# Kernel tuning notes

Hardware: AMD Instinct MI355X
Metric: run time of the kernel (lower is better)

## Reference

```python
import jax, jax.numpy as jnp
import numpy as np

EPS = 1e-5

def setup_inputs() -> dict:
    key = jax.random.key(0)
    ks = jax.random.split(key, 8)
    N, C, ST, LT = 32, 2048, 16, 400
    ALPHA, K, BETA, CK = 4, 3, 4, 3
    Cb = C // BETA
    inp = {
        'st_feat': jax.random.normal(ks[0], (N, C, ST, 1, 1), dtype=jnp.float32),
        'lt_feat': jax.random.normal(ks[1], (N, C, LT, 1, 1), dtype=jnp.float32),
        # global branch G: Linear(ST->ST*alpha) -> BN1d -> ReLU -> Linear(->K) -> softmax
        'g_w1': jax.random.normal(ks[2], (ST * ALPHA, ST), dtype=jnp.float32) * 0.02,
        'g_bn_gamma': jnp.ones((ST * ALPHA,), jnp.float32),
        'g_bn_beta': jnp.zeros((ST * ALPHA,), jnp.float32),
        'g_bn_mean': jnp.zeros((ST * ALPHA,), jnp.float32),
        'g_bn_var': jnp.ones((ST * ALPHA,), jnp.float32),
        'g_w2': jax.random.normal(ks[3], (K, ST * ALPHA), dtype=jnp.float32) * 0.02,
        # local branch L: Conv1d(C->C/beta,k=3) -> BN1d -> ReLU -> Conv1d(C/beta->C,1) -> sigmoid
        'l_w1': jax.random.normal(ks[4], (Cb, C, CK), dtype=jnp.float32) * 0.02,
        'l_bn_gamma': jnp.ones((Cb,), jnp.float32),
        'l_bn_beta': jnp.zeros((Cb,), jnp.float32),
        'l_bn_mean': jnp.zeros((Cb,), jnp.float32),
        'l_bn_var': jnp.ones((Cb,), jnp.float32),
        'l_w2': jax.random.normal(ks[5], (C, Cb), dtype=jnp.float32) * 0.02,
    }
    return inp


def reference(st_feat, lt_feat, g_w1, g_bn_gamma, g_bn_beta, g_bn_mean, g_bn_var,
              g_w2, l_w1, l_bn_gamma, l_bn_beta, l_bn_mean, l_bn_var, l_w2):
    N, C, ST = st_feat.shape[:3]
    LT = lt_feat.shape[2]
    K = g_w2.shape[0]
    PAD = 1  # adaptive_convolution_padding; stride = 1
    # ---- global branch: per-(n,c) adaptive kernel (h=w=1 so avgpool is identity)
    st = st_feat.reshape(N * C, ST)                               # [NC, ST]
    h = st @ g_w1.T                                               # [NC, ST*alpha]
    h = (h - g_bn_mean) * jax.lax.rsqrt(g_bn_var + EPS) * g_bn_gamma + g_bn_beta
    h = jax.nn.relu(h)
    conv_kernel = jax.nn.softmax(h @ g_w2.T, axis=-1)             # [NC, K]
    # ---- local branch: channel-temporal sigmoid gate
    lt = lt_feat.reshape(N, C, LT)                                # [N, C, LT]
    x = jax.lax.conv_general_dilated(lt, l_w1, window_strides=(1,),
                                     padding=[(1, 1)],
                                     dimension_numbers=('NCH', 'OIH', 'NCH'))  # [N, C/beta, LT]
    x = (x - l_bn_mean[None, :, None]) * jax.lax.rsqrt(l_bn_var + EPS)[None, :, None] \
        * l_bn_gamma[None, :, None] + l_bn_beta[None, :, None]
    x = jax.nn.relu(x)
    gate = jax.nn.sigmoid(jnp.einsum('oc,nct->not', l_w2, x))     # [N, C, LT]
    new_lt = lt * gate
    # ---- temporal adaptive aggregation: per-(n,c) depthwise 1D conv, K taps
    kern = conv_kernel.reshape(N, C, K)
    xp = jnp.pad(new_lt, ((0, 0), (0, 0), (PAD, PAD)))            # [N, C, LT+2*PAD]
    out_len = LT + 2 * PAD - K + 1                                # == LT for K=3, PAD=1
    out = jnp.zeros((N, C, out_len), dtype=new_lt.dtype)
    for i in range(K):  # K is tiny (3)
        out = out + kern[:, :, i:i + 1] * xp[:, :, i:i + out_len]
    return out.reshape(N, C, out_len, 1, 1)
```

## Files before the change

### kernel.cpp

```cpp
#include <hip/hip_runtime.h>
#include <hip/hip_bf16.h>

#define N_   32
#define C_   2048
#define ST_  16
#define H_   64
#define K_   3
#define CB_  512
#define LT_  400
#define LTP_ 402
#define BK   32
#define TV1  254

using bf16x8 = __attribute__((ext_vector_type(8))) __bf16;
using f32x4  = __attribute__((ext_vector_type(4))) float;
typedef unsigned short ushort_t;

__device__ __forceinline__ unsigned short f2bf(float f) {
    unsigned int u = __float_as_uint(f);
    u = (u + 0x7fffu + ((u >> 16) & 1u)) >> 16;
    return (unsigned short)u;
}
__device__ __forceinline__ float bf2f(unsigned short h) {
    return __uint_as_float(((unsigned int)h) << 16);
}
__device__ __forceinline__ void gload16(const ushort_t* g, ushort_t* l) {
    __builtin_amdgcn_global_load_lds(
        (const __attribute__((address_space(1))) unsigned int*)g,
        (__attribute__((address_space(3))) unsigned int*)l, 16, 0, 0);
}

__global__ __launch_bounds__(256) void k_global(
    const float* __restrict__ st, const float* __restrict__ g_w1,
    const float* __restrict__ gam, const float* __restrict__ bet,
    const float* __restrict__ mean, const float* __restrict__ var,
    const float* __restrict__ g_w2, float* __restrict__ kern) {
    __shared__ float w1[H_][ST_];
    __shared__ float sc[H_], bi[H_];
    __shared__ float w2[K_][H_];
    int tid = threadIdx.x;
    for (int i = tid; i < H_ * ST_; i += 256) w1[i / ST_][i % ST_] = g_w1[i];
    if (tid < H_) {
        float s = gam[tid] * rsqrtf(var[tid] + 1e-5f);
        sc[tid] = s;
        bi[tid] = bet[tid] - mean[tid] * s;
    }
    for (int i = tid; i < K_ * H_; i += 256) w2[i / H_][i % H_] = g_w2[i];
    __syncthreads();
    int row = blockIdx.x * 256 + tid;
    const float* p = st + (size_t)row * ST_;
    float s[ST_];
#pragma unroll
    for (int i = 0; i < ST_; ++i) s[i] = p[i];
    float lg0 = 0.f, lg1 = 0.f, lg2 = 0.f;
    for (int j = 0; j < H_; ++j) {
        float h = 0.f;
#pragma unroll
        for (int i = 0; i < ST_; ++i) h = fmaf(w1[j][i], s[i], h);
        h = fmaxf(fmaf(h, sc[j], bi[j]), 0.f);
        lg0 = fmaf(w2[0][j], h, lg0);
        lg1 = fmaf(w2[1][j], h, lg1);
        lg2 = fmaf(w2[2][j], h, lg2);
    }
    float m = fmaxf(lg0, fmaxf(lg1, lg2));
    float e0 = __expf(lg0 - m), e1 = __expf(lg1 - m), e2 = __expf(lg2 - m);
    float inv = 1.f / (e0 + e1 + e2);
    float4 o = make_float4(e0 * inv, e1 * inv, e2 * inv, 0.f);
    *(float4*)(kern + (size_t)row * 4) = o;
}

__global__ __launch_bounds__(256) void k_transpose(
    const float* __restrict__ lt, ushort_t* __restrict__ ltT) {
    __shared__ float tile[32][33];
    int tt0 = blockIdx.x * 32;
    int cc  = blockIdx.y * 32;
    int n   = blockIdx.z;
    const float* src = lt + ((size_t)n * C_ + cc) * LT_;
    int tx = threadIdx.x & 31, ty = threadIdx.x >> 5;
#pragma unroll
    for (int i = 0; i < 4; ++i) {
        int c = ty + i * 8;
        int t = tt0 + tx;
        tile[c][tx] = (t < LT_) ? src[(size_t)c * LT_ + t] : 0.f;
    }
    __syncthreads();
    int cx  = (threadIdx.x & 15) * 2;
    int tyw = threadIdx.x >> 4;
    unsigned int* dst = (unsigned int*)(ltT + (size_t)n * LTP_ * C_ + cc + cx);
#pragma unroll
    for (int i = 0; i < 2; ++i) {
        int tl = tyw + i * 16;
        int t = tt0 + tl;
        if (t < LT_) {
            unsigned int v = (unsigned int)f2bf(tile[cx][tl]) |
                             ((unsigned int)f2bf(tile[cx + 1][tl]) << 16);
            dst[(size_t)(t + 1) * (C_ / 2)] = v;
        }
    }
}

__global__ __launch_bounds__(256) void k_zero(ushort_t* __restrict__ ltT) {
    int i = blockIdx.x * 256 + threadIdx.x;
    int n = i >> 11, c = i & (C_ - 1);
    size_t base = (size_t)n * LTP_ * C_;
    ltT[base + c] = 0;
    ltT[base + (size_t)(LTP_ - 1) * C_ + c] = 0;
}

__global__ __launch_bounds__(256) void k_w1(
    const float* __restrict__ l_w1, ushort_t* __restrict__ w1b) {
    int i = blockIdx.x * 256 + threadIdx.x;
    float a = l_w1[(size_t)i * 3 + 0];
    float b = l_w1[(size_t)i * 3 + 1];
    float c = l_w1[(size_t)i * 3 + 2];
    w1b[0 * (size_t)CB_ * C_ + i] = f2bf(a);
    w1b[1 * (size_t)CB_ * C_ + i] = f2bf(b);
    w1b[2 * (size_t)CB_ * C_ + i] = f2bf(c);
}

__global__ __launch_bounds__(256) void k_w2(
    const float* __restrict__ l_w2, ushort_t* __restrict__ w2b) {
    int i = blockIdx.x * 256 + threadIdx.x;
    w2b[i] = f2bf(l_w2[i]);
}

__global__ __launch_bounds__(512, 2) void k_gemm1(
    const ushort_t* __restrict__ ltT, const ushort_t* __restrict__ w1b,
    const float* __restrict__ bn_g, const float* __restrict__ bn_b,
    const float* __restrict__ bn_m, const float* __restrict__ bn_v,
    ushort_t* __restrict__ Xws) {
    __shared__ __align__(16) ushort_t Asm[3 * 256 * BK + 2 * BK];
    __shared__ __align__(16) ushort_t Bsm[3 * 384 * BK];
    const int tid = threadIdx.x;
    const int mseg = blockIdx.x;
    const int n   = mseg >> 1;
    const int tm  = (mseg & 1) * TV1;
    const int cb0 = blockIdx.y * 128;
    const int lane = tid & 63, lrow = lane & 15, quad = lane >> 4;
    const int wv = tid >> 6;
    const int wvM = wv >> 1, wvN = wv & 1;

    const int srow = lane >> 2;
    const int csrc = (((lane & 3) ^ ((lane >> 3) & 3)) << 3);
    const ushort_t* gA[2];
#pragma unroll
    for (int i = 0; i < 2; ++i) {
        int r = (2 * wv + i) * 16 + srow;
        int gr = tm + r; gr = gr < LTP_ - 1 ? gr : LTP_ - 1;
        gA[i] = ltT + ((size_t)n * LTP_ + gr) * C_ + csrc;
    }
    const ushort_t* gB[3];
#pragma unroll
    for (int j = 0; j < 3; ++j) {
        int rB = (3 * wv + j) * 16 + srow;
        gB[j] = w1b + ((size_t)((rB >> 7) * CB_ + cb0 + (rB & 127))) * C_ + csrc;
    }
    const int sB = lrow * BK + ((quad ^ ((lrow >> 1) & 3)) << 3);
    int sA[3];
#pragma unroll
    for (int k = 0; k < 3; ++k)
        sA[k] = (lrow + k) * BK + ((quad ^ (((lrow + k) >> 1) & 3)) << 3);

    f32x4 acc[4][4];
#pragma unroll
    for (int i = 0; i < 4; ++i)
#pragma unroll
        for (int j = 0; j < 4; ++j) acc[i][j] = (f32x4){0.f, 0.f, 0.f, 0.f};

#define STAGE1(buf)                                                         \
    {                                                                       \
        ushort_t* ad = Asm + (buf) * (256 * BK) + (2 * wv) * (16 * BK);     \
        gload16(gA[0], ad);                                                 \
        gload16(gA[1], ad + 16 * BK);                                       \
        gA[0] += BK; gA[1] += BK;                                           \
        ushort_t* bd = Bsm + (buf) * (384 * BK) + (3 * wv) * (16 * BK);     \
        gload16(gB[0], bd);                                                 \
        gload16(gB[1], bd + 16 * BK);                                       \
        gload16(gB[2], bd + 32 * BK);                                       \
        gB[0] += BK; gB[1] += BK; gB[2] += BK;                              \
    }

    STAGE1(0);
    STAGE1(1);
    int cur = 0, pre = 2;
    for (int s = 0; s < C_ / BK; ++s) {
        if (s < C_ / BK - 1) asm volatile("s_waitcnt vmcnt(5)" ::: "memory");
        else                 asm volatile("s_waitcnt vmcnt(0)" ::: "memory");
        __builtin_amdgcn_sched_barrier(0);
        __builtin_amdgcn_s_barrier();
        __builtin_amdgcn_sched_barrier(0);
        if (s < C_ / BK - 2) {
            STAGE1(pre);
            pre = (pre == 2) ? 0 : pre + 1;
        }
        const ushort_t* Ab = Asm + cur * (256 * BK) + wvM * (64 * BK);
        const ushort_t* Bb = Bsm + cur * (384 * BK) + wvN * (64 * BK) + sB;
        bf16x8 bfr[3][4];
#pragma unroll
        for (int k = 0; k < 3; ++k)
#pragma unroll
            for (int nf = 0; nf < 4; ++nf)
                bfr[k][nf] = *(const bf16x8*)(Bb + k * (128 * BK) + nf * (16 * BK));
        __builtin_amdgcn_s_setprio(1);
#pragma unroll
        for (int mf = 0; mf < 4; ++mf) {
            bf16x8 af[3];
#pragma unroll
            for (int k = 0; k < 3; ++k)
                af[k] = *(const bf16x8*)(Ab + sA[k] + mf * (16 * BK));
#pragma unroll
            for (int nf = 0; nf < 4; ++nf)
#pragma unroll
                for (int k = 0; k < 3; ++k)
                    acc[mf][nf] = __builtin_amdgcn_mfma_f32_16x16x32_bf16(af[k], bfr[k][nf], acc[mf][nf], 0, 0, 0);
        }
        __builtin_amdgcn_s_setprio(0);
        cur = (cur == 2) ? 0 : cur + 1;
    }
#undef STAGE1
    float sc[4], bo[4];
#pragma unroll
    for (int nf = 0; nf < 4; ++nf) {
        int cb = cb0 + wvN * 64 + nf * 16 + lrow;
        float s0 = bn_g[cb] * rsqrtf(bn_v[cb] + 1e-5f);
        sc[nf] = s0;
        bo[nf] = bn_b[cb] - bn_m[cb] * s0;
    }
#pragma unroll
    for (int mf = 0; mf < 4; ++mf) {
#pragma unroll
        for (int r = 0; r < 4; ++r) {
            int local = wvM * 64 + mf * 16 + quad * 4 + r;
            int t = tm + local;
            if (local < TV1 && t < LT_) {
#pragma unroll
                for (int nf = 0; nf < 4; ++nf) {
                    int cb = cb0 + wvN * 64 + nf * 16 + lrow;
                    float v = fmaxf(fmaf(acc[mf][nf][r], sc[nf], bo[nf]), 0.f);
                    Xws[((size_t)n * LT_ + t) * CB_ + cb] = f2bf(v);
                }
            }
        }
    }
}

__global__ __launch_bounds__(256, 3) void k_gemm2(
    const ushort_t* __restrict__ Xws, const ushort_t* __restrict__ w2b,
    ushort_t* __restrict__ gate) {
    __shared__ __align__(16) ushort_t Asm[3 * 128 * BK];
    __shared__ __align__(16) ushort_t Bsm[3 * 128 * BK];
    const int tid = threadIdx.x;
    const int cm  = blockIdx.x * 128;
    const int fn0 = blockIdx.y * 128;
    const int lane = tid & 63, lrow = lane & 15, quad = lane >> 4;
    const int wv = tid >> 6, wvM = wv & 1, wvN = wv >> 1;

    const int srow = lane >> 2;
    const int csrc = (((lane & 3) ^ ((lane >> 3) & 3)) << 3);
    const ushort_t* gA[2];
    const ushort_t* gB[2];
#pragma unroll
    for (int i = 0; i < 2; ++i) {
        int r = (2 * wv + i) * 16 + srow;
        gA[i] = w2b + (size_t)(cm + r) * CB_ + csrc;
        gB[i] = Xws + (size_t)(fn0 + r) * CB_ + csrc;
    }
    const int sOff = lrow * BK + ((quad ^ ((lrow >> 1) & 3)) << 3);

    f32x4 acc[4][4];
#pragma unroll
    for (int i = 0; i < 4; ++i)
#pragma unroll
        for (int j = 0; j < 4; ++j) acc[i][j] = (f32x4){0.f, 0.f, 0.f, 0.f};

#define STAGE2(buf)                                                         \
    {                                                                       \
        ushort_t* ad = Asm + (buf) * (128 * BK) + (2 * wv) * (16 * BK);     \
        ushort_t* bd = Bsm + (buf) * (128 * BK) + (2 * wv) * (16 * BK);     \
        gload16(gA[0], ad);                                                 \
        gload16(gA[1], ad + 16 * BK);                                       \
        gload16(gB[0], bd);                                                 \
        gload16(gB[1], bd + 16 * BK);                                       \
        gA[0] += BK; gA[1] += BK; gB[0] += BK; gB[1] += BK;                 \
    }

    STAGE2(0);
    STAGE2(1);
    int cur = 0, pre = 2;
    for (int s = 0; s < CB_ / BK; ++s) {
        if (s < CB_ / BK - 1) asm volatile("s_waitcnt vmcnt(4)" ::: "memory");
        else                  asm volatile("s_waitcnt vmcnt(0)" ::: "memory");
        __builtin_amdgcn_sched_barrier(0);
        __builtin_amdgcn_s_barrier();
        __builtin_amdgcn_sched_barrier(0);
        if (s < CB_ / BK - 2) {
            STAGE2(pre);
            pre = (pre == 2) ? 0 : pre + 1;
        }
        const ushort_t* Ab = Asm + cur * (128 * BK) + wvM * (64 * BK) + sOff;
        const ushort_t* Bb = Bsm + cur * (128 * BK) + wvN * (64 * BK) + sOff;
        bf16x8 af[4], bfm[4];
#pragma unroll
        for (int mf = 0; mf < 4; ++mf)
            af[mf] = *(const bf16x8*)(Ab + mf * (16 * BK));
#pragma unroll
        for (int nf = 0; nf < 4; ++nf)
            bfm[nf] = *(const bf16x8*)(Bb + nf * (16 * BK));
        __builtin_amdgcn_s_setprio(1);
#pragma unroll
        for (int mf = 0; mf < 4; ++mf)
#pragma unroll
            for (int nf = 0; nf < 4; ++nf)
                acc[mf][nf] = __builtin_amdgcn_mfma_f32_16x16x32_bf16(af[mf], bfm[nf], acc[mf][nf], 0, 0, 0);
        __builtin_amdgcn_s_setprio(0);
        cur = (cur == 2) ? 0 : cur + 1;
    }
#undef STAGE2
#pragma unroll
    for (int mf = 0; mf < 4; ++mf) {
#pragma unroll
        for (int r = 0; r < 4; ++r) {
            int c = cm + wvM * 64 + mf * 16 + quad * 4 + r;
#pragma unroll
            for (int nf = 0; nf < 4; ++nf) {
                unsigned fn = fn0 + wvN * 64 + nf * 16 + lrow;
                unsigned nn = fn / LT_;
                unsigned t  = fn - nn * LT_;
                float g = 1.f / (1.f + __expf(-acc[mf][nf][r]));
                gate[((size_t)nn * C_ + c) * LT_ + t] = f2bf(g);
            }
        }
    }
}

__global__ __launch_bounds__(256) void k_final(
    const float* __restrict__ lt, const ushort_t* __restrict__ gate,
    const float* __restrict__ kern, float* __restrict__ out) {
    long long idx = (long long)blockIdx.x * 256 + threadIdx.x;
    int t0 = (int)(idx % 50) * 8;
    long long nc = idx / 50;
    const float*    ltp = lt   + (size_t)nc * LT_;
    const ushort_t* gp  = gate + (size_t)nc * LT_;
    float4 kv = *(const float4*)(kern + (size_t)nc * 4);
    float4 va = *(const float4*)(ltp + t0);
    float4 vb = *(const float4*)(ltp + t0 + 4);
    float lm = (t0 > 0) ? ltp[t0 - 1] : 0.f;
    float lp = (t0 + 8 < LT_) ? ltp[t0 + 8] : 0.f;
    uint2 ga = *(const uint2*)(gp + t0);
    uint2 gb = *(const uint2*)(gp + t0 + 4);
    unsigned short gm = (t0 > 0) ? gp[t0 - 1] : (unsigned short)0;
    unsigned short gq = (t0 + 8 < LT_) ? gp[t0 + 8] : (unsigned short)0;
    float nl[10];
    nl[0] = lm   * bf2f(gm);
    nl[1] = va.x * bf2f((unsigned short)(ga.x & 0xffffu));
    nl[2] = va.y * bf2f((unsigned short)(ga.x >> 16));
    nl[3] = va.z * bf2f((unsigned short)(ga.y & 0xffffu));
    nl[4] = va.w * bf2f((unsigned short)(ga.y >> 16));
    nl[5] = vb.x * bf2f((unsigned short)(gb.x & 0xffffu));
    nl[6] = vb.y * bf2f((unsigned short)(gb.x >> 16));
    nl[7] = vb.z * bf2f((unsigned short)(gb.y & 0xffffu));
    nl[8] = vb.w * bf2f((unsigned short)(gb.y >> 16));
    nl[9] = lp   * bf2f(gq);
    float4 o0, o1;
    o0.x = kv.x * nl[0] + kv.y * nl[1] + kv.z * nl[2];
    o0.y = kv.x * nl[1] + kv.y * nl[2] + kv.z * nl[3];
    o0.z = kv.x * nl[2] + kv.y * nl[3] + kv.z * nl[4];
    o0.w = kv.x * nl[3] + kv.y * nl[4] + kv.z * nl[5];
    o1.x = kv.x * nl[4] + kv.y * nl[5] + kv.z * nl[6];
    o1.y = kv.x * nl[5] + kv.y * nl[6] + kv.z * nl[7];
    o1.z = kv.x * nl[6] + kv.y * nl[7] + kv.z * nl[8];
    o1.w = kv.x * nl[7] + kv.y * nl[8] + kv.z * nl[9];
    *(float4*)(out + (size_t)nc * LT_ + t0) = o0;
    *(float4*)(out + (size_t)nc * LT_ + t0 + 4) = o1;
}

extern "C" void kernel_launch(void* const* d_in, const int* in_sizes, int n_in,
                              void* d_out, int out_size, void* d_ws, size_t ws_size,
                              hipStream_t stream) {
    const float* st   = (const float*)d_in[0];
    const float* lt   = (const float*)d_in[1];
    const float* g_w1 = (const float*)d_in[2];
    const float* g_bg = (const float*)d_in[3];
    const float* g_bb = (const float*)d_in[4];
    const float* g_bm = (const float*)d_in[5];
    const float* g_bv = (const float*)d_in[6];
    const float* g_w2 = (const float*)d_in[7];
    const float* l_w1 = (const float*)d_in[8];
    const float* l_bg = (const float*)d_in[9];
    const float* l_bb = (const float*)d_in[10];
    const float* l_bm = (const float*)d_in[11];
    const float* l_bv = (const float*)d_in[12];
    const float* l_w2 = (const float*)d_in[13];
    float* out = (float*)d_out;

    char* ws = (char*)d_ws;
    float*    kern = (float*)(ws + 0);
    ushort_t* w1b  = (ushort_t*)(ws + 1048576);
    ushort_t* w2b  = (ushort_t*)(ws + 7340032);
    ushort_t* Xws  = (ushort_t*)(ws + 9437184);
    ushort_t* ltT  = (ushort_t*)(ws + 22544384);
    ushort_t* gate = ltT;

    k_global<<<dim3((N_ * C_) / 256), dim3(256), 0, stream>>>(
        st, g_w1, g_bg, g_bb, g_bm, g_bv, g_w2, kern);
    k_w1<<<dim3((CB_ * C_) / 256), dim3(256), 0, stream>>>(l_w1, w1b);
    k_w2<<<dim3((C_ * CB_) / 256), dim3(256), 0, stream>>>(l_w2, w2b);
    k_zero<<<dim3((N_ * C_) / 256), dim3(256), 0, stream>>>(ltT);
    k_transpose<<<dim3(13, C_ / 32, N_), dim3(256), 0, stream>>>(lt, ltT);
    k_gemm1<<<dim3(64, 4), dim3(512), 0, stream>>>(
        ltT, w1b, l_bg, l_bb, l_bm, l_bv, Xws);
    k_gemm2<<<dim3(C_ / 128, 100), dim3(256), 0, stream>>>(Xws, w2b, gate);
    k_final<<<dim3((N_ * C_ * 50) / 256), dim3(256), 0, stream>>>(
        lt, gate, kern, out);
}
```

Measured before the change: 433.1 us.

## Fuse gating and temporal depthwise conv into second GEMM epilogue with halo tiles

Removes the separate final kernel and the bf16 gate buffer by computing sigmoid gate, multiplying by lt, and applying the 3-tap per-channel conv directly in the GEMM2 epilogue. Column tiles are overlapped by one element on each side (126 useful of 128) so neighbors come from lane shuffles plus a small shared-memory exchange across waves. This removes the gate write and re-read, but adds about 1.6% extra GEMM tiles, block-wide syncs in the epilogue, and strided uncoalesced lt loads and out stores.

```diff
diff --git a/kernel.cpp b/kernel.cpp
--- a/kernel.cpp
+++ b/kernel.cpp
@@ -11,6 +11,8 @@
 #define LTP_ 402
 #define BK   32
 #define TV1  254
+#define FNT  12800
+#define JW   126
 
 using bf16x8 = __attribute__((ext_vector_type(8))) __bf16;
 using f32x4  = __attribute__((ext_vector_type(4))) float;
@@ -246,12 +248,14 @@
 
 __global__ __launch_bounds__(256, 3) void k_gemm2(
     const ushort_t* __restrict__ Xws, const ushort_t* __restrict__ w2b,
-    ushort_t* __restrict__ gate) {
+    const float* __restrict__ lt, const float* __restrict__ kern,
+    float* __restrict__ out) {
     __shared__ __align__(16) ushort_t Asm[3 * 128 * BK];
     __shared__ __align__(16) ushort_t Bsm[3 * 128 * BK];
+    __shared__ float nbnd[128][2];
     const int tid = threadIdx.x;
     const int cm  = blockIdx.x * 128;
-    const int fn0 = blockIdx.y * 128;
+    const int fnBase = (int)blockIdx.y * JW - 1;
     const int lane = tid & 63, lrow = lane & 15, quad = lane >> 4;
     const int wv = tid >> 6, wvM = wv & 1, wvN = wv >> 1;
 
@@ -263,7 +267,9 @@
     for (int i = 0; i < 2; ++i) {
         int r = (2 * wv + i) * 16 + srow;
         gA[i] = w2b + (size_t)(cm + r) * CB_ + csrc;
-        gB[i] = Xws + (size_t)(fn0 + r) * CB_ + csrc;
+        int fr = fnBase + r;
+        fr = fr < 0 ? 0 : (fr > FNT - 1 ? FNT - 1 : fr);
+        gB[i] = Xws + (size_t)fr * CB_ + csrc;
     }
     const int sOff = lrow * BK + ((quad ^ ((lrow >> 1) & 3)) << 3);
 
@@ -318,60 +324,70 @@
 #undef STAGE2
 #pragma unroll
     for (int mf = 0; mf < 4; ++mf) {
+        int cl = wvM * 64 + mf * 16 + quad * 4;
+        int c4 = cm + cl;
+        f32x4 nlv[4];
+#pragma unroll
+        for (int nf = 0; nf < 4; ++nf) {
+            int j  = wvN * 64 + nf * 16 + lrow;
+            int fn = fnBase + j;
+            int fnc = fn < 0 ? 0 : (fn > FNT - 1 ? FNT - 1 : fn);
+            int nn = fnc / LT_, t = fnc - nn * LT_;
+            const float* ltp = lt + ((size_t)nn * C_ + c4) * LT_ + t;
+#pragma unroll
+            for (int r = 0; r < 4; ++r) {
+                float g = 1.f / (1.f + __expf(-acc[mf][nf][r]));
+                nlv[nf][r] = ltp[(size_t)r * LT_] * g;
+            }
+        }
+        if (wvN == 0 && lrow == 15) {
+#pragma unroll
+            for (int r = 0; r < 4; ++r) nbnd[cl + r][0] = nlv[3][r];
+        }
+        if (wvN == 1 && lrow == 0) {
+#pragma unroll
+            for (int r = 0; r < 4; ++r) nbnd[cl + r][1] = nlv[0][r];
+        }
+        __syncthreads();
 #pragma unroll
         for (int r = 0; r < 4; ++r) {
-            int c = cm + wvM * 64 + mf * 16 + quad * 4 + r;
+            int c = c4 + r;
+            float v0 = nlv[0][r], v1 = nlv[1][r], v2 = nlv[2][r], v3 = nlv[3][r];
+            float u0 = __shfl(v0, lane + 1, 64), x1 = __shfl(v1, lane - 15, 64);
+            float u1 = __shfl(v1, lane + 1, 64), x2 = __shfl(v2, lane - 15, 64);
+            float u2 = __shfl(v2, lane + 1, 64), x3 = __shfl(v3, lane - 15, 64);
+            float u3 = __shfl(v3, lane + 1, 64);
+            float r0 = (lrow < 15) ? u0 : x1;
+            float r1 = (lrow < 15) ? u1 : x2;
+            float r2 = (lrow < 15) ? u2 : x3;
+            float r3 = (lrow < 15) ? u3 : ((wvN == 0) ? nbnd[cl + r][1] : 0.f);
+            float d0 = __shfl(v0, lane - 1, 64), y0 = __shfl(v0, lane + 15, 64);
+            float d1 = __shfl(v1, lane - 1, 64), y1 = __shfl(v1, lane + 15, 64);
+            float d2 = __shfl(v2, lane - 1, 64), y2 = __shfl(v2, lane + 15, 64);
+            float d3 = __shfl(v3, lane - 1, 64);
+            float l0 = (lrow > 0) ? d0 : ((wvN == 1) ? nbnd[cl + r][0] : 0.f);
+            float l1 = (lrow > 0) ? d1 : y0;
+            float l2 = (lrow > 0) ? d2 : y1;
+            float l3 = (lrow > 0) ? d3 : y2;
+            float ctr[4] = {v0, v1, v2, v3};
+            float lft[4] = {l0, l1, l2, l3};
+            float rgt[4] = {r0, r1, r2, r3};
 #pragma unroll
             for (int nf = 0; nf < 4; ++nf) {
-                unsigned fn = fn0 + wvN * 64 + nf * 16 + lrow;
-                unsigned nn = fn / LT_;
-                unsigned t  = fn - nn * LT_;
-                float g = 1.f / (1.f + __expf(-acc[mf][nf][r]));
-                gate[((size_t)nn * C_ + c) * LT_ + t] = f2bf(g);
+                int j  = wvN * 64 + nf * 16 + lrow;
+                int fn = fnBase + j;
+                if (j >= 1 && j <= JW && fn < FNT) {
+                    int nn = fn / LT_, t = fn - nn * LT_;
+                    float4 kv = *(const float4*)(kern + ((size_t)nn * C_ + c) * 4);
+                    float o = kv.y * ctr[nf];
+                    if (t > 0)       o += kv.x * lft[nf];
+                    if (t < LT_ - 1) o += kv.z * rgt[nf];
+                    out[((size_t)nn * C_ + c) * LT_ + t] = o;
+                }
             }
         }
-    }
-}
-
-__global__ __launch_bounds__(256) void k_final(
-    const float* __restrict__ lt, const ushort_t* __restrict__ gate,
-    const float* __restrict__ kern, float* __restrict__ out) {
-    long long idx = (long long)blockIdx.x * 256 + threadIdx.x;
-    int t0 = (int)(idx % 50) * 8;
-    long long nc = idx / 50;
-    const float*    ltp = lt   + (size_t)nc * LT_;
-    const ushort_t* gp  = gate + (size_t)nc * LT_;
-    float4 kv = *(const float4*)(kern + (size_t)nc * 4);
-    float4 va = *(const float4*)(ltp + t0);
-    float4 vb = *(const float4*)(ltp + t0 + 4);
-    float lm = (t0 > 0) ? ltp[t0 - 1] : 0.f;
-    float lp = (t0 + 8 < LT_) ? ltp[t0 + 8] : 0.f;
-    uint2 ga = *(const uint2*)(gp + t0);
-    uint2 gb = *(const uint2*)(gp + t0 + 4);
-    unsigned short gm = (t0 > 0) ? gp[t0 - 1] : (unsigned short)0;
-    unsigned short gq = (t0 + 8 < LT_) ? gp[t0 + 8] : (unsigned short)0;
-    float nl[10];
-    nl[0] = lm   * bf2f(gm);
-    nl[1] = va.x * bf2f((unsigned short)(ga.x & 0xffffu));
-    nl[2] = va.y * bf2f((unsigned short)(ga.x >> 16));
-    nl[3] = va.z * bf2f((unsigned short)(ga.y & 0xffffu));
-    nl[4] = va.w * bf2f((unsigned short)(ga.y >> 16));
-    nl[5] = vb.x * bf2f((unsigned short)(gb.x & 0xffffu));
-    nl[6] = vb.y * bf2f((unsigned short)(gb.x >> 16));
-    nl[7] = vb.z * bf2f((unsigned short)(gb.y & 0xffffu));
-    nl[8] = vb.w * bf2f((unsigned short)(gb.y >> 16));
-    nl[9] = lp   * bf2f(gq);
-    float4 o0, o1;
-    o0.x = kv.x * nl[0] + kv.y * nl[1] + kv.z * nl[2];
-    o0.y = kv.x * nl[1] + kv.y * nl[2] + kv.z * nl[3];
-    o0.z = kv.x * nl[2] + kv.y * nl[3] + kv.z * nl[4];
-    o0.w = kv.x * nl[3] + kv.y * nl[4] + kv.z * nl[5];
-    o1.x = kv.x * nl[4] + kv.y * nl[5] + kv.z * nl[6];
-    o1.y = kv.x * nl[5] + kv.y * nl[6] + kv.z * nl[7];
-    o1.z = kv.x * nl[6] + kv.y * nl[7] + kv.z * nl[8];
-    o1.w = kv.x * nl[7] + kv.y * nl[8] + kv.z * nl[9];
-    *(float4*)(out + (size_t)nc * LT_ + t0) = o0;
-    *(float4*)(out + (size_t)nc * LT_ + t0 + 4) = o1;
+        __syncthreads();
+    }
 }
 
 extern "C" void kernel_launch(void* const* d_in, const int* in_sizes, int n_in,
@@ -399,7 +415,6 @@
     ushort_t* w2b  = (ushort_t*)(ws + 7340032);
     ushort_t* Xws  = (ushort_t*)(ws + 9437184);
     ushort_t* ltT  = (ushort_t*)(ws + 22544384);
-    ushort_t* gate = ltT;
 
     k_global<<<dim3((N_ * C_) / 256), dim3(256), 0, stream>>>(
         st, g_w1, g_bg, g_bb, g_bm, g_bv, g_w2, kern);
@@ -409,7 +424,6 @@
     k_transpose<<<dim3(13, C_ / 32, N_), dim3(256), 0, stream>>>(lt, ltT);
     k_gemm1<<<dim3(64, 4), dim3(512), 0, stream>>>(
         ltT, w1b, l_bg, l_bb, l_bm, l_bv, Xws);
-    k_gemm2<<<dim3(C_ / 128, 100), dim3(256), 0, stream>>>(Xws, w2b, gate);
-    k_final<<<dim3((N_ * C_ * 50) / 256), dim3(256), 0, stream>>>(
-        lt, gate, kern, out);
-}
+    k_gemm2<<<dim3(C_ / 128, (FNT + JW - 1) / JW), dim3(256), 0, stream>>>(
+        Xws, w2b, lt, kern, out);
+}
```

Result: slower. 455.0 us (+5.0%).
